# Kernel tuning notes

Hardware: AMD Instinct MI355X
Metric: run time of the kernel (lower is better)

The kernel has to match this reference:

```python
import jax, jax.numpy as jnp
import numpy as np

B = 16384
N_DENSE = 13
N_TABLES = 26
VOCAB = 100000
DIM = 64
BOTTOM_DIMS = [13, 512, 256, 64]
TOP_DIMS = [442, 512, 256, 1]
TOP_SIGMOID_POS = 2  # sigmoid on last top layer; bottom uses relu everywhere


def _init_mlp(key, dims, scale=0.05):
    ws, bs = [], []
    for i in range(len(dims) - 1):
        key, k = jax.random.split(key)
        ws.append(jax.random.normal(k, (dims[i], dims[i + 1]), dtype=jnp.float32) * scale)
        bs.append(jnp.zeros((dims[i + 1],), dtype=jnp.float32))
    return ws, bs


def setup_inputs() -> dict:
    key = jax.random.key(0)
    k_dense, k_sparse, k_tab, k_b, k_t = jax.random.split(key, 5)
    dense_inputs = jax.random.normal(k_dense, (B, N_DENSE), dtype=jnp.float32)
    sparse_inputs = jax.random.randint(k_sparse, (B, N_TABLES), 0, VOCAB, dtype=jnp.int64)
    tables = jax.random.normal(k_tab, (N_TABLES, VOCAB, DIM), dtype=jnp.float32) * 0.01
    bws, bbs = _init_mlp(k_b, BOTTOM_DIMS)
    tws, tbs = _init_mlp(k_t, TOP_DIMS)
    return {
        'dense_inputs': dense_inputs, 'sparse_inputs': sparse_inputs, 'tables': tables,
        'bw1': bws[0], 'bb1': bbs[0], 'bw2': bws[1], 'bb2': bbs[1], 'bw3': bws[2], 'bb3': bbs[2],
        'tw1': tws[0], 'tb1': tbs[0], 'tw2': tws[1], 'tb2': tbs[1], 'tw3': tws[2], 'tb3': tbs[2],
    }


def _mlp(x, ws, bs, sigmoid_pos):
    for i, (w, b) in enumerate(zip(ws, bs)):
        x = x @ w + b
        x = jax.nn.sigmoid(x) if (sigmoid_pos is not None and i == sigmoid_pos) else jax.nn.relu(x)
    return x


def reference(dense_inputs, sparse_inputs, tables,
              bw1, bb1, bw2, bb2, bw3, bb3,
              tw1, tb1, tw2, tb2, tw3, tb3):
    # Bottom MLP: [B,13] -> [B,64], relu on every layer
    dx = _mlp(dense_inputs, [bw1, bw2, bw3], [bb1, bb2, bb3], None)
    # Multi-table embedding gather: [B,26] -> [B,26,64]
    sx = tables[jnp.arange(N_TABLES)[None, :], sparse_inputs]
    # Dot interaction (self_interaction=True): stack dense + sparse fields
    T = jnp.concatenate([dx[:, None, :], sx], axis=1)          # [B, 27, 64]
    Z = jnp.einsum('bfd,bgd->bfg', T, T)                        # [B, 27, 27]
    F = N_TABLES + 1
    iu, ju = jnp.triu_indices(F, k=0)                           # include diagonal
    flat = Z[:, iu, ju]                                         # [B, 378]
    interaction = jnp.concatenate([dx, flat], axis=1)           # [B, 442]
    # Top MLP with sigmoid on the last layer
    return _mlp(interaction, [tw1, tw2, tw3], [tb1, tb2, tb3], TOP_SIGMOID_POS)
```

## Files before the change

### kernel.cpp

```cpp
#include <hip/hip_runtime.h>

typedef unsigned short u16;
typedef _Float16 f16;
typedef __attribute__((ext_vector_type(8))) _Float16 half8;
typedef __attribute__((ext_vector_type(4))) float f32x4;
typedef __attribute__((ext_vector_type(16))) float f32x16;

#define DEV __device__ __forceinline__

static constexpr int BATCH   = 16384;
static constexpr int NTAB    = 26;
static constexpr int VOCAB   = 100000;
static constexpr int DIM     = 64;

DEV u16 f2h(float f){ union { f16 h; u16 u; } x; x.h = (f16)f; return x.u; }

DEV void llds16(u16* dst, const u16* src){
  __builtin_amdgcn_global_load_lds(
      (const __attribute__((address_space(1))) unsigned*)src,
      (__attribute__((address_space(3))) unsigned*)dst, 16, 0, 0);
}

DEV int crow(int reg, int half){ return (reg & 3) + 8 * (reg >> 2) + 4 * half; }

DEV void wtile(const float* __restrict__ src, u16* __restrict__ dst,
               int K, int N, int Kpad, int tile)
{
  __shared__ float ld[32][33];
  const int nt = N >> 5;
  const int k0 = (tile / nt) << 5;
  const int n0 = (tile % nt) << 5;
  const int tx = threadIdx.x & 31;
  const int ty = threadIdx.x >> 5;
  #pragma unroll
  for (int it = 0; it < 4; ++it) {
    int k = k0 + ty + 8 * it;
    ld[ty + 8 * it][tx] = (k < K) ? src[(size_t)k * N + n0 + tx] : 0.f;
  }
  __syncthreads();
  #pragma unroll
  for (int it = 0; it < 4; ++it) {
    int n  = n0 + ty + 8 * it;
    int kp = k0 + tx;
    dst[(size_t)n * Kpad + kp] = f2h(ld[tx][ty + 8 * it]);
  }
}

__global__ void prep_k(const float* __restrict__ dense, u16* __restrict__ Xs,
                       const float* __restrict__ bw1, u16* __restrict__ W1s,
                       const float* __restrict__ bw2, u16* __restrict__ W2s,
                       const float* __restrict__ bw3, u16* __restrict__ W3s,
                       const float* __restrict__ tw1, u16* __restrict__ WT1s,
                       const float* __restrict__ tw2, u16* __restrict__ WT2s)
{
  int blk = blockIdx.x;
  if (blk < 2048) {
    int i = blk * 256 + threadIdx.x;
    int b = i >> 5, k = i & 31;
    float v = (k < 13) ? dense[b * 13 + k] : 0.f;
    Xs[(size_t)b * 32 + k] = f2h(v);
  }
  else if (blk < 2064) wtile(bw1, W1s, 13, 512, 32,    blk - 2048);
  else if (blk < 2192) wtile(bw2, W2s, 512, 256, 512,  blk - 2064);
  else if (blk < 2208) wtile(bw3, W3s, 256, 64, 256,   blk - 2192);
  else if (blk < 2464) wtile(tw1, WT1s, 442, 512, 512, blk - 2208);
  else                 wtile(tw2, WT2s, 512, 256, 512, blk - 2464);
}

__global__ __launch_bounds__(512)
void bottom_mlp_k(const u16* __restrict__ Xs, const u16* __restrict__ W1s,
                  const u16* __restrict__ W2s, const u16* __restrict__ W3s,
                  const float* __restrict__ bb1, const float* __restrict__ bb2,
                  const float* __restrict__ bb3, float* __restrict__ dxf)
{
  __shared__ alignas(16) u16 lds[67584];
  u16* A1  = lds;
  u16* S   = lds + 32768;
  u16* Xl  = S;
  u16* W1l = S + 2048;
  u16* W2b0 = S + 18432;
  u16* W2b1 = S;
  u16* A2  = S + 18432;
  u16* W3l = S;

  const int tid = threadIdx.x, lane = tid & 63, wid = tid >> 6;
  int bid = blockIdx.x;
  bid = (bid & 7) * 32 + (bid >> 3);
  const int m0  = bid * 64;
  const int l31 = lane & 31, half = lane >> 5;

  auto stageW2 = [&](int t, u16* buf) {
    #pragma unroll
    for (int it = 0; it < 4; ++it) {
      int loff = (it * 512 + tid) * 16;
      int row  = loff >> 7, slot = (loff & 127) >> 4, gs = slot ^ (row & 7);
      llds16(buf + (size_t)(it * 512 + (wid << 6)) * 8,
             W2s + (size_t)row * 512 + t * 64 + gs * 8);
    }
  };

  if (tid < 256) {
    int loff = tid * 16, row = loff >> 6, slot = (loff & 63) >> 4, gs = slot ^ (row & 3);
    llds16(Xl + (size_t)(wid << 6) * 8, Xs + (size_t)(m0 + row) * 32 + gs * 8);
  }
  #pragma unroll
  for (int it = 0; it < 4; ++it) {
    int loff = (it * 512 + tid) * 16, row = loff >> 6, slot = (loff & 63) >> 4,
        gs = slot ^ (row & 3);
    llds16(W1l + (size_t)(it * 512 + (wid << 6)) * 8, W1s + (size_t)row * 32 + gs * 8);
  }
  stageW2(0, W2b0);
  asm volatile("s_waitcnt vmcnt(4)" ::: "memory");
  __builtin_amdgcn_s_barrier();

  f32x16 acc1[2][2] = {};
  #pragma unroll
  for (int ks = 0; ks < 2; ++ks) {
    half8 af[2], bf[2];
    #pragma unroll
    for (int mi = 0; mi < 2; ++mi) {
      int row = mi * 32 + l31, sl = (2 * ks + half) ^ (row & 3);
      af[mi] = *(const half8*)(Xl + (size_t)row * 32 + sl * 8);
    }
    #pragma unroll
    for (int ni = 0; ni < 2; ++ni) {
      int row = wid * 64 + ni * 32 + l31, sl = (2 * ks + half) ^ (row & 3);
      bf[ni] = *(const half8*)(W1l + (size_t)row * 32 + sl * 8);
    }
    #pragma unroll
    for (int mi = 0; mi < 2; ++mi)
      #pragma unroll
      for (int ni = 0; ni < 2; ++ni)
        acc1[mi][ni] = __builtin_amdgcn_mfma_f32_32x32x16_f16(af[mi], bf[ni], acc1[mi][ni], 0, 0, 0);
  }
  #pragma unroll
  for (int ni = 0; ni < 2; ++ni) {
    int col = wid * 64 + ni * 32 + l31;
    float bv = bb1[col];
    #pragma unroll
    for (int mi = 0; mi < 2; ++mi)
      #pragma unroll
      for (int reg = 0; reg < 16; ++reg) {
        int row = mi * 32 + crow(reg, half);
        float v = fmaxf(acc1[mi][ni][reg] + bv, 0.f);
        A1[(size_t)row * 512 + (((col >> 3) ^ (row & 63)) * 8) + (col & 7)] = f2h(v);
      }
  }
  __syncthreads();

  f32x16 acc2[2] = {};
  for (int t = 0; t < 8; ++t) {
    asm volatile("s_waitcnt vmcnt(0)" ::: "memory");
    __builtin_amdgcn_s_barrier();
    if (t < 7) stageW2(t + 1, ((t + 1) & 1) ? W2b1 : W2b0);
    const u16* buf = (t & 1) ? W2b1 : W2b0;
    #pragma unroll
    for (int ks = 0; ks < 4; ++ks) {
      int s = t * 4 + ks;
      half8 af[2], bf;
      #pragma unroll
      for (int mi = 0; mi < 2; ++mi) {
        int row = mi * 32 + l31, sl = (2 * s + half) ^ (row & 63);
        af[mi] = *(const half8*)(A1 + (size_t)row * 512 + sl * 8);
      }
      {
        int row = wid * 32 + l31, sl = (2 * ks + half) ^ (row & 7);
        bf = *(const half8*)(buf + (size_t)row * 64 + sl * 8);
      }
      #pragma unroll
      for (int mi = 0; mi < 2; ++mi)
        acc2[mi] = __builtin_amdgcn_mfma_f32_32x32x16_f16(af[mi], bf, acc2[mi], 0, 0, 0);
    }
  }
  {
    int col = wid * 32 + l31;
    float bv = bb2[col];
    #pragma unroll
    for (int mi = 0; mi < 2; ++mi)
      #pragma unroll
      for (int reg = 0; reg < 16; ++reg) {
        int row = mi * 32 + crow(reg, half);
        float v = fmaxf(acc2[mi][reg] + bv, 0.f);
        A2[(size_t)row * 256 + (((col >> 3) ^ (row & 31)) * 8) + (col & 7)] = f2h(v);
      }
  }
  __syncthreads();

  #pragma unroll
  for (int it = 0; it < 4; ++it) {
    int loff = (it * 512 + tid) * 16;
    int row = loff >> 9, slot = (loff & 511) >> 4, gs = slot ^ (row & 31);
    llds16(W3l + (size_t)(it * 512 + (wid << 6)) * 8, W3s + (size_t)row * 256 + gs * 8);
  }
  asm volatile("s_waitcnt vmcnt(0)" ::: "memory");
  __builtin_amdgcn_s_barrier();

  if (wid < 4) {
    f32x16 acc3 = {};
    const int gm = (wid >> 1) * 32, gn = (wid & 1) * 32;
    #pragma unroll
    for (int s = 0; s < 16; ++s) {
      int rowa = gm + l31, sa = (2 * s + half) ^ (rowa & 31);
      half8 a = *(const half8*)(A2 + (size_t)rowa * 256 + sa * 8);
      int rowb = gn + l31, sb = (2 * s + half) ^ (rowb & 31);
      half8 b = *(const half8*)(W3l + (size_t)rowb * 256 + sb * 8);
      acc3 = __builtin_amdgcn_mfma_f32_32x32x16_f16(a, b, acc3, 0, 0, 0);
    }
    #pragma unroll
    for (int reg = 0; reg < 16; ++reg) {
      int col = gn + l31, row = gm + crow(reg, half);
      dxf[(size_t)(m0 + row) * 64 + col] = fmaxf(acc3[reg] + bb3[col], 0.f);
    }
  }
}

__global__ __launch_bounds__(256)
void interact_k(const float* __restrict__ dxf, const int* __restrict__ sidx,
                const float* __restrict__ tables, u16* __restrict__ Is)
{
  const int lane = threadIdx.x & 63;
  const int b    = blockIdx.x * 4 + (threadIdx.x >> 6);
  const float* dxrow = dxf + (size_t)b * DIM;
  u16* irow = Is + (size_t)b * 512;

  irow[lane] = f2h(dxrow[lane]);
  irow[442 + lane] = 0;
  if (lane < 6) irow[506 + lane] = 0;

  const int r    = lane & 31;
  const int half = lane >> 5;
  const float* src = nullptr;
  if (r == 0)       src = dxrow;
  else if (r <= 26) {
    int id = sidx[b * NTAB + (r - 1)];
    src = tables + ((size_t)(r - 1) * VOCAB + (size_t)id) * DIM;
  }

  half8 fh[4];
  #pragma unroll
  for (int ks = 0; ks < 4; ++ks) {
    half8 h = {};
    if (src) {
      const float* p = src + ks * 16 + half * 8;
      f32x4 a = *(const f32x4*)(p);
      f32x4 c = *(const f32x4*)(p + 4);
      #pragma unroll
      for (int j = 0; j < 4; ++j) { h[j] = (f16)a[j]; h[j + 4] = (f16)c[j]; }
    }
    fh[ks] = h;
  }

  f32x16 z = {};
  #pragma unroll
  for (int ks = 0; ks < 4; ++ks)
    z = __builtin_amdgcn_mfma_f32_32x32x16_f16(fh[ks], fh[ks], z, 0, 0, 0);

  const int col = r;
  if (col < 27) {
    #pragma unroll
    for (int reg = 0; reg < 16; ++reg) {
      int rw = crow(reg, half);
      if (rw <= col) {
        int flat = rw * 27 - rw * (rw - 1) / 2 + (col - rw);
        irow[64 + flat] = f2h(z[reg]);
      }
    }
  }
}

__global__ __launch_bounds__(512)
void top_mlp_k(const u16* __restrict__ Is, const u16* __restrict__ WT1s,
               const u16* __restrict__ WT2s, const float* __restrict__ tb1,
               const float* __restrict__ tb2, const float* __restrict__ tw3,
               const float* __restrict__ tb3, float* __restrict__ out)
{
  __shared__ alignas(16) u16 lds[65536];
  __shared__ float redbuf[8][64];
  u16* AB  = lds;
  u16* Wb0 = lds + 32768;
  u16* Wb1 = lds + 49152;

  const int tid = threadIdx.x, lane = tid & 63, wid = tid >> 6;
  int bid = blockIdx.x;
  bid = (bid & 7) * 32 + (bid >> 3);
  const int m0  = bid * 64;
  const int l31 = lane & 31, half = lane >> 5;

  auto stageW4 = [&](int t, u16* buf) {
    #pragma unroll
    for (int it = 0; it < 4; ++it) {
      int p  = (it * 512 + tid) * 16;
      int pr = p >> 7, ps = (p & 127) >> 4;
      int un = ps ^ (pr & 7);
      int row = 2 * pr + (un >> 2), ls = un & 3;
      llds16(buf + (size_t)(it * 512 + (wid << 6)) * 8,
             WT1s + (size_t)row * 512 + t * 32 + ls * 8);
    }
  };
  auto stageW5 = [&](int t, u16* buf) {
    #pragma unroll
    for (int it = 0; it < 4; ++it) {
      int loff = (it * 512 + tid) * 16;
      int row = loff >> 7, slot = (loff & 127) >> 4, gs = slot ^ (row & 7);
      llds16(buf + (size_t)(it * 512 + (wid << 6)) * 8,
             WT2s + (size_t)row * 512 + t * 64 + gs * 8);
    }
  };

  #pragma unroll
  for (int it = 0; it < 8; ++it) {
    int loff = (it * 512 + tid) * 16;
    int row = loff >> 10, slot = (loff & 1023) >> 4, gs = slot ^ (row & 63);
    llds16(AB + (size_t)(it * 512 + (wid << 6)) * 8,
           Is + (size_t)(m0 + row) * 512 + gs * 8);
  }
  stageW4(0, Wb0);

  f32x16 acc4[2][2] = {};
  for (int t = 0; t < 16; ++t) {
    asm volatile("s_waitcnt vmcnt(0)" ::: "memory");
    __builtin_amdgcn_s_barrier();
    if (t < 15) stageW4(t + 1, ((t + 1) & 1) ? Wb1 : Wb0);
    const u16* buf = (t & 1) ? Wb1 : Wb0;
    #pragma unroll
    for (int ks = 0; ks < 2; ++ks) {
      int s = t * 2 + ks;
      half8 af[2], bf[2];
      #pragma unroll
      for (int mi = 0; mi < 2; ++mi) {
        int row = mi * 32 + l31, sl = (2 * s + half) ^ (row & 63);
        af[mi] = *(const half8*)(AB + (size_t)row * 512 + sl * 8);
      }
      #pragma unroll
      for (int ni = 0; ni < 2; ++ni) {
        int n = wid * 64 + ni * 32 + l31;
        int pr = n >> 1;
        int ps = (4 * (n & 1) + 2 * ks + half) ^ (pr & 7);
        bf[ni] = *(const half8*)(buf + (size_t)pr * 64 + ps * 8);
      }
      #pragma unroll
      for (int mi = 0; mi < 2; ++mi)
        #pragma unroll
        for (int ni = 0; ni < 2; ++ni)
          acc4[mi][ni] = __builtin_amdgcn_mfma_f32_32x32x16_f16(af[mi], bf[ni], acc4[mi][ni], 0, 0, 0);
    }
  }
  __syncthreads();
  #pragma unroll
  for (int ni = 0; ni < 2; ++ni) {
    int col = wid * 64 + ni * 32 + l31;
    float bv = tb1[col];
    #pragma unroll
    for (int mi = 0; mi < 2; ++mi)
      #pragma unroll
      for (int reg = 0; reg < 16; ++reg) {
        int row = mi * 32 + crow(reg, half);
        float v = fmaxf(acc4[mi][ni][reg] + bv, 0.f);
        AB[(size_t)row * 512 + (((col >> 3) ^ (row & 63)) * 8) + (col & 7)] = f2h(v);
      }
  }
  __syncthreads();

  stageW5(0, Wb0);
  f32x16 acc5[2] = {};
  for (int t = 0; t < 8; ++t) {
    asm volatile("s_waitcnt vmcnt(0)" ::: "memory");
    __builtin_amdgcn_s_barrier();
    if (t < 7) stageW5(t + 1, ((t + 1) & 1) ? Wb1 : Wb0);
    const u16* buf = (t & 1) ? Wb1 : Wb0;
    #pragma unroll
    for (int ks = 0; ks < 4; ++ks) {
      int s = t * 4 + ks;
      half8 af[2], bf;
      #pragma unroll
      for (int mi = 0; mi < 2; ++mi) {
        int row = mi * 32 + l31, sl = (2 * s + half) ^ (row & 63);
        af[mi] = *(const half8*)(AB + (size_t)row * 512 + sl * 8);
      }
      {
        int row = wid * 32 + l31, sl = (2 * ks + half) ^ (row & 7);
        bf = *(const half8*)(buf + (size_t)row * 64 + sl * 8);
      }
      #pragma unroll
      for (int mi = 0; mi < 2; ++mi)
        acc5[mi] = __builtin_amdgcn_mfma_f32_32x32x16_f16(af[mi], bf, acc5[mi], 0, 0, 0);
    }
  }
  {
    int col = wid * 32 + l31;
    float bv = tb2[col], wv = tw3[col];
    #pragma unroll
    for (int mi = 0; mi < 2; ++mi)
      #pragma unroll
      for (int reg = 0; reg < 16; ++reg) {
        float s = fmaxf(acc5[mi][reg] + bv, 0.f) * wv;
        #pragma unroll
        for (int off = 16; off; off >>= 1) s += __shfl_xor(s, off);
        if (l31 == 0) redbuf[wid][mi * 32 + crow(reg, half)] = s;
      }
  }
  __syncthreads();
  if (tid < 64) {
    float s = tb3[0];
    #pragma unroll
    for (int w = 0; w < 8; ++w) s += redbuf[w][tid];
    out[m0 + tid] = 1.f / (1.f + expf(-s));
  }
}

extern "C" void kernel_launch(void* const* d_in, const int* in_sizes, int n_in,
                              void* d_out, int out_size, void* d_ws, size_t ws_size,
                              hipStream_t stream)
{
  const float* dense  = (const float*)d_in[0];
  const int*   sidx   = (const int*)d_in[1];
  const float* tables = (const float*)d_in[2];
  const float* bw1 = (const float*)d_in[3];  const float* bb1 = (const float*)d_in[4];
  const float* bw2 = (const float*)d_in[5];  const float* bb2 = (const float*)d_in[6];
  const float* bw3 = (const float*)d_in[7];  const float* bb3 = (const float*)d_in[8];
  const float* tw1 = (const float*)d_in[9];  const float* tb1 = (const float*)d_in[10];
  const float* tw2 = (const float*)d_in[11]; const float* tb2 = (const float*)d_in[12];
  const float* tw3 = (const float*)d_in[13]; const float* tb3 = (const float*)d_in[14];
  float* out = (float*)d_out;

  char* ws = (char*)d_ws;
  size_t off = 0;
  auto alloc = [&](size_t bytes) { size_t o = off; off += (bytes + 1023) & ~(size_t)1023; return o; };

  u16*  Xs   = (u16*)(ws + alloc((size_t)BATCH * 32 * 2));
  u16*  W1s  = (u16*)(ws + alloc((size_t)512 * 32 * 2));
  u16*  W2s  = (u16*)(ws + alloc((size_t)256 * 512 * 2));
  u16*  W3s  = (u16*)(ws + alloc((size_t)64 * 256 * 2));
  u16*  WT1s = (u16*)(ws + alloc((size_t)512 * 512 * 2));
  u16*  WT2s = (u16*)(ws + alloc((size_t)256 * 512 * 2));
  float* dxf = (float*)(ws + alloc((size_t)BATCH * 64 * 4));
  u16*  Is   = (u16*)(ws + alloc((size_t)BATCH * 512 * 2));
  (void)ws_size; (void)n_in; (void)in_sizes; (void)out_size;

  prep_k<<<2592, 256, 0, stream>>>(dense, Xs, bw1, W1s, bw2, W2s, bw3, W3s,
                                   tw1, WT1s, tw2, WT2s);
  bottom_mlp_k<<<256, 512, 0, stream>>>(Xs, W1s, W2s, W3s, bb1, bb2, bb3, dxf);
  interact_k<<<BATCH / 4, 256, 0, stream>>>(dxf, sidx, tables, Is);
  top_mlp_k<<<256, 512, 0, stream>>>(Is, WT1s, WT2s, tb1, tb2, tw3, tb3, out);
}
```

Measured before the change: 74.92 us.

## Fuse bottom MLP, interaction, and top MLP into one kernel

Merges the bottom MLP, embedding gather with dot interaction, and top MLP into a single 256-block kernel. The dense features and the interaction row stay in LDS instead of going through global dxf and Is buffers. The embedding gathers are software-pipelined per wave with double register buffers. This removes two launches and the global round-trips, but the gather phase now runs on only 256 blocks with fewer waves in flight to hide random-access latency, and LDS use grows.

```diff
diff --git a/kernel.cpp b/kernel.cpp
--- a/kernel.cpp
+++ b/kernel.cpp
@@ -68,20 +68,28 @@
 }
 
 __global__ __launch_bounds__(512)
-void bottom_mlp_k(const u16* __restrict__ Xs, const u16* __restrict__ W1s,
-                  const u16* __restrict__ W2s, const u16* __restrict__ W3s,
-                  const float* __restrict__ bb1, const float* __restrict__ bb2,
-                  const float* __restrict__ bb3, float* __restrict__ dxf)
+void mega_k(const u16* __restrict__ Xs, const u16* __restrict__ W1s,
+            const u16* __restrict__ W2s, const u16* __restrict__ W3s,
+            const float* __restrict__ bb1, const float* __restrict__ bb2,
+            const float* __restrict__ bb3, const int* __restrict__ sidx,
+            const float* __restrict__ tables, const u16* __restrict__ WT1s,
+            const u16* __restrict__ WT2s, const float* __restrict__ tb1,
+            const float* __restrict__ tb2, const float* __restrict__ tw3,
+            const float* __restrict__ tb3, float* __restrict__ out)
 {
-  __shared__ alignas(16) u16 lds[67584];
-  u16* A1  = lds;
-  u16* S   = lds + 32768;
-  u16* Xl  = S;
-  u16* W1l = S + 2048;
-  u16* W2b0 = S + 18432;
-  u16* W2b1 = S;
-  u16* A2  = S + 18432;
-  u16* W3l = S;
+  __shared__ alignas(16) u16 lds[71680];
+  __shared__ float redbuf[8][64];
+  u16* AB   = lds;
+  u16* R1   = lds + 32768;
+  u16* Xl   = R1;
+  u16* W1l  = R1 + 2048;
+  u16* W2b0 = R1 + 18432;
+  u16* W2b1 = R1;
+  u16* A2   = R1 + 18432;
+  u16* W3l  = R1;
+  u16* dxl  = R1 + 34816;
+  u16* Wb0  = R1;
+  u16* Wb1  = R1 + 16384;
 
   const int tid = threadIdx.x, lane = tid & 63, wid = tid >> 6;
   int bid = blockIdx.x;
@@ -113,66 +121,68 @@
   asm volatile("s_waitcnt vmcnt(4)" ::: "memory");
   __builtin_amdgcn_s_barrier();
 
-  f32x16 acc1[2][2] = {};
-  #pragma unroll
-  for (int ks = 0; ks < 2; ++ks) {
-    half8 af[2], bf[2];
-    #pragma unroll
-    for (int mi = 0; mi < 2; ++mi) {
-      int row = mi * 32 + l31, sl = (2 * ks + half) ^ (row & 3);
-      af[mi] = *(const half8*)(Xl + (size_t)row * 32 + sl * 8);
+  {
+    f32x16 acc1[2][2] = {};
+    #pragma unroll
+    for (int ks = 0; ks < 2; ++ks) {
+      half8 af[2], bf[2];
+      #pragma unroll
+      for (int mi = 0; mi < 2; ++mi) {
+        int row = mi * 32 + l31, sl = (2 * ks + half) ^ (row & 3);
+        af[mi] = *(const half8*)(Xl + (size_t)row * 32 + sl * 8);
+      }
+      #pragma unroll
+      for (int ni = 0; ni < 2; ++ni) {
+        int row = wid * 64 + ni * 32 + l31, sl = (2 * ks + half) ^ (row & 3);
+        bf[ni] = *(const half8*)(W1l + (size_t)row * 32 + sl * 8);
+      }
+      #pragma unroll
+      for (int mi = 0; mi < 2; ++mi)
+        #pragma unroll
+        for (int ni = 0; ni < 2; ++ni)
+          acc1[mi][ni] = __builtin_amdgcn_mfma_f32_32x32x16_f16(af[mi], bf[ni], acc1[mi][ni], 0, 0, 0);
     }
     #pragma unroll
     for (int ni = 0; ni < 2; ++ni) {
-      int row = wid * 64 + ni * 32 + l31, sl = (2 * ks + half) ^ (row & 3);
-      bf[ni] = *(const half8*)(W1l + (size_t)row * 32 + sl * 8);
-    }
-    #pragma unroll
-    for (int mi = 0; mi < 2; ++mi)
-      #pragma unroll
-      for (int ni = 0; ni < 2; ++ni)
-        acc1[mi][ni] = __builtin_amdgcn_mfma_f32_32x32x16_f16(af[mi], bf[ni], acc1[mi][ni], 0, 0, 0);
-  }
-  #pragma unroll
-  for (int ni = 0; ni < 2; ++ni) {
-    int col = wid * 64 + ni * 32 + l31;
-    float bv = bb1[col];
-    #pragma unroll
-    for (int mi = 0; mi < 2; ++mi)
-      #pragma unroll
-      for (int reg = 0; reg < 16; ++reg) {
-        int row = mi * 32 + crow(reg, half);
-        float v = fmaxf(acc1[mi][ni][reg] + bv, 0.f);
-        A1[(size_t)row * 512 + (((col >> 3) ^ (row & 63)) * 8) + (col & 7)] = f2h(v);
-      }
-  }
-  __syncthreads();
-
-  f32x16 acc2[2] = {};
-  for (int t = 0; t < 8; ++t) {
-    asm volatile("s_waitcnt vmcnt(0)" ::: "memory");
-    __builtin_amdgcn_s_barrier();
-    if (t < 7) stageW2(t + 1, ((t + 1) & 1) ? W2b1 : W2b0);
-    const u16* buf = (t & 1) ? W2b1 : W2b0;
-    #pragma unroll
-    for (int ks = 0; ks < 4; ++ks) {
-      int s = t * 4 + ks;
-      half8 af[2], bf;
-      #pragma unroll
-      for (int mi = 0; mi < 2; ++mi) {
-        int row = mi * 32 + l31, sl = (2 * s + half) ^ (row & 63);
-        af[mi] = *(const half8*)(A1 + (size_t)row * 512 + sl * 8);
-      }
-      {
-        int row = wid * 32 + l31, sl = (2 * ks + half) ^ (row & 7);
-        bf = *(const half8*)(buf + (size_t)row * 64 + sl * 8);
-      }
+      int col = wid * 64 + ni * 32 + l31;
+      float bv = bb1[col];
       #pragma unroll
       for (int mi = 0; mi < 2; ++mi)
-        acc2[mi] = __builtin_amdgcn_mfma_f32_32x32x16_f16(af[mi], bf, acc2[mi], 0, 0, 0);
-    }
-  }
+        #pragma unroll
+        for (int reg = 0; reg < 16; ++reg) {
+          int row = mi * 32 + crow(reg, half);
+          float v = fmaxf(acc1[mi][ni][reg] + bv, 0.f);
+          AB[(size_t)row * 512 + (((col >> 3) ^ (row & 63)) * 8) + (col & 7)] = f2h(v);
+        }
+    }
+  }
+  __syncthreads();
+
   {
+    f32x16 acc2[2] = {};
+    for (int t = 0; t < 8; ++t) {
+      asm volatile("s_waitcnt vmcnt(0)" ::: "memory");
+      __builtin_amdgcn_s_barrier();
+      if (t < 7) stageW2(t + 1, ((t + 1) & 1) ? W2b1 : W2b0);
+      const u16* buf = (t & 1) ? W2b1 : W2b0;
+      #pragma unroll
+      for (int ks = 0; ks < 4; ++ks) {
+        int s = t * 4 + ks;
+        half8 af[2], bf;
+        #pragma unroll
+        for (int mi = 0; mi < 2; ++mi) {
+          int row = mi * 32 + l31, sl = (2 * s + half) ^ (row & 63);
+          af[mi] = *(const half8*)(AB + (size_t)row * 512 + sl * 8);
+        }
+        {
+          int row = wid * 32 + l31, sl = (2 * ks + half) ^ (row & 7);
+          bf = *(const half8*)(buf + (size_t)row * 64 + sl * 8);
+        }
+        #pragma unroll
+        for (int mi = 0; mi < 2; ++mi)
+          acc2[mi] = __builtin_amdgcn_mfma_f32_32x32x16_f16(af[mi], bf, acc2[mi], 0, 0, 0);
+      }
+    }
     int col = wid * 32 + l31;
     float bv = bb2[col];
     #pragma unroll
@@ -209,82 +219,11 @@
     #pragma unroll
     for (int reg = 0; reg < 16; ++reg) {
       int col = gn + l31, row = gm + crow(reg, half);
-      dxf[(size_t)(m0 + row) * 64 + col] = fmaxf(acc3[reg] + bb3[col], 0.f);
-    }
-  }
-}
-
-__global__ __launch_bounds__(256)
-void interact_k(const float* __restrict__ dxf, const int* __restrict__ sidx,
-                const float* __restrict__ tables, u16* __restrict__ Is)
-{
-  const int lane = threadIdx.x & 63;
-  const int b    = blockIdx.x * 4 + (threadIdx.x >> 6);
-  const float* dxrow = dxf + (size_t)b * DIM;
-  u16* irow = Is + (size_t)b * 512;
-
-  irow[lane] = f2h(dxrow[lane]);
-  irow[442 + lane] = 0;
-  if (lane < 6) irow[506 + lane] = 0;
-
-  const int r    = lane & 31;
-  const int half = lane >> 5;
-  const float* src = nullptr;
-  if (r == 0)       src = dxrow;
-  else if (r <= 26) {
-    int id = sidx[b * NTAB + (r - 1)];
-    src = tables + ((size_t)(r - 1) * VOCAB + (size_t)id) * DIM;
-  }
-
-  half8 fh[4];
-  #pragma unroll
-  for (int ks = 0; ks < 4; ++ks) {
-    half8 h = {};
-    if (src) {
-      const float* p = src + ks * 16 + half * 8;
-      f32x4 a = *(const f32x4*)(p);
-      f32x4 c = *(const f32x4*)(p + 4);
-      #pragma unroll
-      for (int j = 0; j < 4; ++j) { h[j] = (f16)a[j]; h[j + 4] = (f16)c[j]; }
-    }
-    fh[ks] = h;
-  }
-
-  f32x16 z = {};
-  #pragma unroll
-  for (int ks = 0; ks < 4; ++ks)
-    z = __builtin_amdgcn_mfma_f32_32x32x16_f16(fh[ks], fh[ks], z, 0, 0, 0);
-
-  const int col = r;
-  if (col < 27) {
-    #pragma unroll
-    for (int reg = 0; reg < 16; ++reg) {
-      int rw = crow(reg, half);
-      if (rw <= col) {
-        int flat = rw * 27 - rw * (rw - 1) / 2 + (col - rw);
-        irow[64 + flat] = f2h(z[reg]);
-      }
-    }
-  }
-}
-
-__global__ __launch_bounds__(512)
-void top_mlp_k(const u16* __restrict__ Is, const u16* __restrict__ WT1s,
-               const u16* __restrict__ WT2s, const float* __restrict__ tb1,
-               const float* __restrict__ tb2, const float* __restrict__ tw3,
-               const float* __restrict__ tb3, float* __restrict__ out)
-{
-  __shared__ alignas(16) u16 lds[65536];
-  __shared__ float redbuf[8][64];
-  u16* AB  = lds;
-  u16* Wb0 = lds + 32768;
-  u16* Wb1 = lds + 49152;
-
-  const int tid = threadIdx.x, lane = tid & 63, wid = tid >> 6;
-  int bid = blockIdx.x;
-  bid = (bid & 7) * 32 + (bid >> 3);
-  const int m0  = bid * 64;
-  const int l31 = lane & 31, half = lane >> 5;
+      float v = fmaxf(acc3[reg] + bb3[col], 0.f);
+      dxl[(size_t)row * 64 + (((col >> 3) ^ (row & 7)) * 8) + (col & 7)] = f2h(v);
+    }
+  }
+  __syncthreads();
 
   auto stageW4 = [&](int t, u16* buf) {
     #pragma unroll
@@ -297,6 +236,75 @@
              WT1s + (size_t)row * 512 + t * 32 + ls * 8);
     }
   };
+  stageW4(0, Wb0);
+
+  const int r = l31;
+  auto gload = [&](int sr, f32x4* buf) {
+    if (r >= 1 && r <= 26) {
+      int id = sidx[(size_t)(m0 + sr) * NTAB + (r - 1)];
+      const float* src = tables + ((size_t)(r - 1) * VOCAB + (size_t)id) * DIM;
+      #pragma unroll
+      for (int ks = 0; ks < 4; ++ks) {
+        const float* p = src + ks * 16 + half * 8;
+        buf[2 * ks]     = *(const f32x4*)(p);
+        buf[2 * ks + 1] = *(const f32x4*)(p + 4);
+      }
+    }
+  };
+  auto gram = [&](int sr, const f32x4* buf) {
+    {
+      u16 dv = dxl[(size_t)sr * 64 + (((lane >> 3) ^ (sr & 7)) * 8) + (lane & 7)];
+      AB[(size_t)sr * 512 + (((lane >> 3) ^ (sr & 63)) * 8) + (lane & 7)] = dv;
+      int c = 442 + lane;
+      AB[(size_t)sr * 512 + (((c >> 3) ^ (sr & 63)) * 8) + (c & 7)] = 0;
+      if (lane < 6) {
+        int c2 = 506 + lane;
+        AB[(size_t)sr * 512 + (((c2 >> 3) ^ (sr & 63)) * 8) + (c2 & 7)] = 0;
+      }
+    }
+    half8 fh[4];
+    #pragma unroll
+    for (int ks = 0; ks < 4; ++ks) {
+      half8 h = {};
+      if (r == 0) {
+        int sl = (2 * ks + half) ^ (sr & 7);
+        h = *(const half8*)(dxl + (size_t)sr * 64 + sl * 8);
+      } else if (r <= 26) {
+        f32x4 a = buf[2 * ks], c = buf[2 * ks + 1];
+        #pragma unroll
+        for (int j = 0; j < 4; ++j) { h[j] = (f16)a[j]; h[j + 4] = (f16)c[j]; }
+      }
+      fh[ks] = h;
+    }
+    f32x16 z = {};
+    #pragma unroll
+    for (int ks = 0; ks < 4; ++ks)
+      z = __builtin_amdgcn_mfma_f32_32x32x16_f16(fh[ks], fh[ks], z, 0, 0, 0);
+    if (r < 27) {
+      #pragma unroll
+      for (int reg = 0; reg < 16; ++reg) {
+        int rw = crow(reg, half);
+        if (rw <= r) {
+          int c = 64 + rw * 27 - rw * (rw - 1) / 2 + (r - rw);
+          AB[(size_t)sr * 512 + (((c >> 3) ^ (sr & 63)) * 8) + (c & 7)] = f2h(z[reg]);
+        }
+      }
+    }
+  };
+
+  {
+    f32x4 bufA[8], bufB[8];
+    gload(wid * 8 + 0, bufA);
+    #pragma unroll
+    for (int jj = 0; jj < 8; jj += 2) {
+      if (jj + 1 < 8) gload(wid * 8 + jj + 1, bufB);
+      gram(wid * 8 + jj, bufA);
+      if (jj + 2 < 8) gload(wid * 8 + jj + 2, bufA);
+      if (jj + 1 < 8) gram(wid * 8 + jj + 1, bufB);
+    }
+  }
+  __syncthreads();
+
   auto stageW5 = [&](int t, u16* buf) {
     #pragma unroll
     for (int it = 0; it < 4; ++it) {
@@ -307,86 +315,79 @@
     }
   };
 
-  #pragma unroll
-  for (int it = 0; it < 8; ++it) {
-    int loff = (it * 512 + tid) * 16;
-    int row = loff >> 10, slot = (loff & 1023) >> 4, gs = slot ^ (row & 63);
-    llds16(AB + (size_t)(it * 512 + (wid << 6)) * 8,
-           Is + (size_t)(m0 + row) * 512 + gs * 8);
-  }
-  stageW4(0, Wb0);
-
-  f32x16 acc4[2][2] = {};
-  for (int t = 0; t < 16; ++t) {
-    asm volatile("s_waitcnt vmcnt(0)" ::: "memory");
-    __builtin_amdgcn_s_barrier();
-    if (t < 15) stageW4(t + 1, ((t + 1) & 1) ? Wb1 : Wb0);
-    const u16* buf = (t & 1) ? Wb1 : Wb0;
-    #pragma unroll
-    for (int ks = 0; ks < 2; ++ks) {
-      int s = t * 2 + ks;
-      half8 af[2], bf[2];
-      #pragma unroll
-      for (int mi = 0; mi < 2; ++mi) {
-        int row = mi * 32 + l31, sl = (2 * s + half) ^ (row & 63);
-        af[mi] = *(const half8*)(AB + (size_t)row * 512 + sl * 8);
-      }
-      #pragma unroll
-      for (int ni = 0; ni < 2; ++ni) {
-        int n = wid * 64 + ni * 32 + l31;
-        int pr = n >> 1;
-        int ps = (4 * (n & 1) + 2 * ks + half) ^ (pr & 7);
-        bf[ni] = *(const half8*)(buf + (size_t)pr * 64 + ps * 8);
-      }
+  {
+    f32x16 acc4[2][2] = {};
+    for (int t = 0; t < 16; ++t) {
+      asm volatile("s_waitcnt vmcnt(0)" ::: "memory");
+      __builtin_amdgcn_s_barrier();
+      if (t < 15) stageW4(t + 1, ((t + 1) & 1) ? Wb1 : Wb0);
+      const u16* buf = (t & 1) ? Wb1 : Wb0;
+      #pragma unroll
+      for (int ks = 0; ks < 2; ++ks) {
+        int s = t * 2 + ks;
+        half8 af[2], bf[2];
+        #pragma unroll
+        for (int mi = 0; mi < 2; ++mi) {
+          int row = mi * 32 + l31, sl = (2 * s + half) ^ (row & 63);
+          af[mi] = *(const half8*)(AB + (size_t)row * 512 + sl * 8);
+        }
+        #pragma unroll
+        for (int ni = 0; ni < 2; ++ni) {
+          int n = wid * 64 + ni * 32 + l31;
+          int pr = n >> 1;
+          int ps = (4 * (n & 1) + 2 * ks + half) ^ (pr & 7);
+          bf[ni] = *(const half8*)(buf + (size_t)pr * 64 + ps * 8);
+        }
+        #pragma unroll
+        for (int mi = 0; mi < 2; ++mi)
+          #pragma unroll
+          for (int ni = 0; ni < 2; ++ni)
+            acc4[mi][ni] = __builtin_amdgcn_mfma_f32_32x32x16_f16(af[mi], bf[ni], acc4[mi][ni], 0, 0, 0);
+      }
+    }
+    __syncthreads();
+    #pragma unroll
+    for (int ni = 0; ni < 2; ++ni) {
+      int col = wid * 64 + ni * 32 + l31;
+      float bv = tb1[col];
       #pragma unroll
       for (int mi = 0; mi < 2; ++mi)
         #pragma unroll
-        for (int ni = 0; ni < 2; ++ni)
-          acc4[mi][ni] = __builtin_amdgcn_mfma_f32_32x32x16_f16(af[mi], bf[ni], acc4[mi][ni], 0, 0, 0);
-    }
-  }
-  __syncthreads();
-  #pragma unroll
-  for (int ni = 0; ni < 2; ++ni) {
-    int col = wid * 64 + ni * 32 + l31;
-    float bv = tb1[col];
-    #pragma unroll
-    for (int mi = 0; mi < 2; ++mi)
-      #pragma unroll
-      for (int reg = 0; reg < 16; ++reg) {
-        int row = mi * 32 + crow(reg, half);
-        float v = fmaxf(acc4[mi][ni][reg] + bv, 0.f);
-        AB[(size_t)row * 512 + (((col >> 3) ^ (row & 63)) * 8) + (col & 7)] = f2h(v);
-      }
-  }
-  __syncthreads();
-
-  stageW5(0, Wb0);
-  f32x16 acc5[2] = {};
-  for (int t = 0; t < 8; ++t) {
-    asm volatile("s_waitcnt vmcnt(0)" ::: "memory");
-    __builtin_amdgcn_s_barrier();
-    if (t < 7) stageW5(t + 1, ((t + 1) & 1) ? Wb1 : Wb0);
-    const u16* buf = (t & 1) ? Wb1 : Wb0;
-    #pragma unroll
-    for (int ks = 0; ks < 4; ++ks) {
-      int s = t * 4 + ks;
-      half8 af[2], bf;
-      #pragma unroll
-      for (int mi = 0; mi < 2; ++mi) {
-        int row = mi * 32 + l31, sl = (2 * s + half) ^ (row & 63);
-        af[mi] = *(const half8*)(AB + (size_t)row * 512 + sl * 8);
-      }
-      {
-        int row = wid * 32 + l31, sl = (2 * ks + half) ^ (row & 7);
-        bf = *(const half8*)(buf + (size_t)row * 64 + sl * 8);
-      }
-      #pragma unroll
-      for (int mi = 0; mi < 2; ++mi)
-        acc5[mi] = __builtin_amdgcn_mfma_f32_32x32x16_f16(af[mi], bf, acc5[mi], 0, 0, 0);
-    }
-  }
+        for (int reg = 0; reg < 16; ++reg) {
+          int row = mi * 32 + crow(reg, half);
+          float v = fmaxf(acc4[mi][ni][reg] + bv, 0.f);
+          AB[(size_t)row * 512 + (((col >> 3) ^ (row & 63)) * 8) + (col & 7)] = f2h(v);
+        }
+    }
+  }
+  __syncthreads();
+
   {
+    stageW5(0, Wb0);
+    f32x16 acc5[2] = {};
+    for (int t = 0; t < 8; ++t) {
+      asm volatile("s_waitcnt vmcnt(0)" ::: "memory");
+      __builtin_amdgcn_s_barrier();
+      if (t < 7) stageW5(t + 1, ((t + 1) & 1) ? Wb1 : Wb0);
+      const u16* buf = (t & 1) ? Wb1 : Wb0;
+      #pragma unroll
+      for (int ks = 0; ks < 4; ++ks) {
+        int s = t * 4 + ks;
+        half8 af[2], bf;
+        #pragma unroll
+        for (int mi = 0; mi < 2; ++mi) {
+          int row = mi * 32 + l31, sl = (2 * s + half) ^ (row & 63);
+          af[mi] = *(const half8*)(AB + (size_t)row * 512 + sl * 8);
+        }
+        {
+          int row = wid * 32 + l31, sl = (2 * ks + half) ^ (row & 7);
+          bf = *(const half8*)(buf + (size_t)row * 64 + sl * 8);
+        }
+        #pragma unroll
+        for (int mi = 0; mi < 2; ++mi)
+          acc5[mi] = __builtin_amdgcn_mfma_f32_32x32x16_f16(af[mi], bf, acc5[mi], 0, 0, 0);
+      }
+    }
     int col = wid * 32 + l31;
     float bv = tb2[col], wv = tw3[col];
     #pragma unroll
@@ -433,13 +434,10 @@
   u16*  W3s  = (u16*)(ws + alloc((size_t)64 * 256 * 2));
   u16*  WT1s = (u16*)(ws + alloc((size_t)512 * 512 * 2));
   u16*  WT2s = (u16*)(ws + alloc((size_t)256 * 512 * 2));
-  float* dxf = (float*)(ws + alloc((size_t)BATCH * 64 * 4));
-  u16*  Is   = (u16*)(ws + alloc((size_t)BATCH * 512 * 2));
   (void)ws_size; (void)n_in; (void)in_sizes; (void)out_size;
 
   prep_k<<<2592, 256, 0, stream>>>(dense, Xs, bw1, W1s, bw2, W2s, bw3, W3s,
                                    tw1, WT1s, tw2, WT2s);
-  bottom_mlp_k<<<256, 512, 0, stream>>>(Xs, W1s, W2s, W3s, bb1, bb2, bb3, dxf);
-  interact_k<<<BATCH / 4, 256, 0, stream>>>(dxf, sidx, tables, Is);
-  top_mlp_k<<<256, 512, 0, stream>>>(Is, WT1s, WT2s, tb1, tb2, tw3, tb3, out);
+  mega_k<<<256, 512, 0, stream>>>(Xs, W1s, W2s, W3s, bb1, bb2, bb3, sidx, tables,
+                                  WT1s, WT2s, tb1, tb2, tw3, tb3, out);
 }
```

Result: faster. 68.84 us (-8.1%).
